# Optimization experiments

Measured on AMD Instinct MI355X. Metric: run time of the kernel, lower is better.

The kernel has to match this reference:

```python
import jax, jax.numpy as jnp
import numpy as np

N = 50000
E = 500000
F_IN = 128
H = 128
HEADS = 3
C = 10
G = 64
EPS = 1e-5
NEG_SLOPE = 0.2


def setup_inputs() -> dict:
    key = jax.random.key(0)
    ks = jax.random.split(key, 20)
    s = 0.1
    inp = {
        "x": jax.random.normal(ks[0], (N, F_IN), dtype=jnp.float32),
        "edge_index": jax.random.randint(ks[1], (2, E), 0, N, dtype=jnp.int64),
        "batch": jnp.sort(jax.random.randint(ks[2], (N,), 0, G, dtype=jnp.int64)),
        # GCNConv: lin weight + bias
        "W1": jax.random.normal(ks[3], (F_IN, H), dtype=jnp.float32) * s,
        "b1": jax.random.normal(ks[4], (H,), dtype=jnp.float32) * s,
        "gamma1": jnp.ones((H,), jnp.float32),
        "beta1": jnp.zeros((H,), jnp.float32),
        # SAGEConv: lin_l (neighbors, with bias) + lin_r (root, no bias)
        "Wl": jax.random.normal(ks[5], (H, H), dtype=jnp.float32) * s,
        "bl": jax.random.normal(ks[6], (H,), dtype=jnp.float32) * s,
        "Wr": jax.random.normal(ks[7], (H, H), dtype=jnp.float32) * s,
        "gamma2": jnp.ones((H,), jnp.float32),
        "beta2": jnp.zeros((H,), jnp.float32),
        # GATConv(heads=3, concat=False): lin + attention vectors + bias
        "W3": jax.random.normal(ks[8], (H, HEADS * H), dtype=jnp.float32) * s,
        "att_src": jax.random.normal(ks[9], (HEADS, H), dtype=jnp.float32) * s,
        "att_dst": jax.random.normal(ks[10], (HEADS, H), dtype=jnp.float32) * s,
        "b3": jax.random.normal(ks[11], (H,), dtype=jnp.float32) * s,
        "gamma3": jnp.ones((H,), jnp.float32),
        "beta3": jnp.zeros((H,), jnp.float32),
        # classifier
        "Wc": jax.random.normal(ks[12], (H, C), dtype=jnp.float32) * s,
        "bc": jax.random.normal(ks[13], (C,), dtype=jnp.float32) * s,
    }
    return inp


def _add_self_loops(src, dst):
    loop = jnp.arange(N, dtype=src.dtype)
    return jnp.concatenate([src, loop]), jnp.concatenate([dst, loop])


def _batch_norm(h, gamma, beta):
    mu = h.mean(axis=0)
    var = ((h - mu) ** 2).mean(axis=0)  # biased var, as torch BN training
    return (h - mu) * jax.lax.rsqrt(var + EPS) * gamma + beta


def gcn_conv(x, src, dst, W, b):
    s2, d2 = _add_self_loops(src, dst)
    deg = jax.ops.segment_sum(jnp.ones_like(d2, dtype=x.dtype), d2, num_segments=N)
    dinv = jnp.where(deg > 0, jax.lax.rsqrt(deg), 0.0)
    h = x @ W  # [N, H]
    norm = dinv[s2] * dinv[d2]  # [E+N]
    out = jax.ops.segment_sum(h[s2] * norm[:, None], d2, num_segments=N)
    return out + b


def sage_conv(x, src, dst, Wl, bl, Wr):
    # mean aggregation of neighbors + root transform
    deg = jax.ops.segment_sum(jnp.ones_like(dst, dtype=x.dtype), dst, num_segments=N)
    agg = jax.ops.segment_sum(x[src], dst, num_segments=N) / jnp.maximum(deg, 1.0)[:, None]
    return agg @ Wl + bl + x @ Wr


def gat_conv(x, src, dst, W, att_src, att_dst, b):
    s2, d2 = _add_self_loops(src, dst)
    h = (x @ W).reshape(N, HEADS, H)  # [N, heads, H]
    a_src = (h * att_src).sum(-1)  # [N, heads]
    a_dst = (h * att_dst).sum(-1)
    e = jax.nn.leaky_relu(a_src[s2] + a_dst[d2], NEG_SLOPE)  # [E2, heads]
    m = jax.ops.segment_max(e, d2, num_segments=N)  # stable softmax per target
    ex = jnp.exp(e - m[d2])
    denom = jax.ops.segment_sum(ex, d2, num_segments=N)
    alpha = ex / denom[d2]  # self-loops guarantee denom > 0
    out = jax.ops.segment_sum(h[s2] * alpha[:, :, None], d2, num_segments=N)
    return out.mean(axis=1) + b  # concat=False -> mean over heads


def reference(x, edge_index, batch, W1, b1, gamma1, beta1, Wl, bl, Wr,
              gamma2, beta2, W3, att_src, att_dst, b3, gamma3, beta3, Wc, bc):
    src, dst = edge_index[0], edge_index[1]
    h = jax.nn.elu(_batch_norm(gcn_conv(x, src, dst, W1, b1), gamma1, beta1))
    h = jax.nn.elu(_batch_norm(sage_conv(h, src, dst, Wl, bl, Wr), gamma2, beta2))
    h = jax.nn.elu(_batch_norm(gat_conv(h, src, dst, W3, att_src, att_dst, b3), gamma3, beta3))
    # global mean pool over graphs
    cnt = jax.ops.segment_sum(jnp.ones((N,), h.dtype), batch, num_segments=G)
    pooled = jax.ops.segment_sum(h, batch, num_segments=G) / jnp.maximum(cnt, 1.0)[:, None]
    logits = pooled @ Wc + bc
    return pooled, logits
```

## Files before the change

kernel.cpp:

```cpp
#include <hip/hip_runtime.h>
#include <math.h>

#define NN 50000
#define EE 500000
#define HH 128
#define NHEADS 3
#define CC 10
#define GG 64
#define EPSV 1e-5f
#define SLOPE 0.2f

typedef __attribute__((ext_vector_type(8))) short short8;
typedef __attribute__((ext_vector_type(4))) float f32x4;
typedef __attribute__((ext_vector_type(2))) float f32x2;


__device__ __forceinline__ unsigned short f2b(float x) {
    unsigned int u = __builtin_bit_cast(unsigned int, x);
    return (unsigned short)((u + 0x7fffu + ((u >> 16) & 1u)) >> 16);
}
__device__ __forceinline__ unsigned int pack2(float a, float b) {
    return (unsigned int)f2b(a) | ((unsigned int)f2b(b) << 16);
}
__device__ __forceinline__ float2 b2f2(unsigned int u) {
    float2 r;
    r.x = __builtin_bit_cast(float, u << 16);
    r.y = __builtin_bit_cast(float, u & 0xffff0000u);
    return r;
}


__global__ void k_zero(int* __restrict__ deg, float* __restrict__ bn1,
                       float* __restrict__ bn_sums23, float* __restrict__ poolacc) {
    int i = blockIdx.x * 256 + threadIdx.x;
    if (i < NN) deg[i] = 0;
    if (i < 256) bn1[i] = 0.f;
    if (i < 512) bn_sums23[i] = 0.f;
    if (i < GG * 128 + GG) poolacc[i] = 0.f;
}


__global__ void k_count_deg(const int* __restrict__ ei, int* __restrict__ deg) {
    int e = blockIdx.x * 256 + threadIdx.x;
    if (e < EE) atomicAdd(&deg[ei[EE + e]], 1);
}

__global__ void k_scan1(const int* __restrict__ deg, int* __restrict__ row_start,
                        int* __restrict__ blk) {
    __shared__ int s[256];
    int i = blockIdx.x * 256 + threadIdx.x;
    int v = (i < NN) ? deg[i] : 0;
    s[threadIdx.x] = v;
    __syncthreads();
    for (int o = 1; o < 256; o <<= 1) {
        int t = (threadIdx.x >= o) ? s[threadIdx.x - o] : 0;
        __syncthreads();
        s[threadIdx.x] += t;
        __syncthreads();
    }
    if (i < NN) row_start[i] = s[threadIdx.x] - v;
    if (threadIdx.x == 255) blk[blockIdx.x] = s[255];
}

__global__ void k_scan2(int* __restrict__ blk, int nb) {
    __shared__ int s[256];
    int v = (threadIdx.x < nb) ? blk[threadIdx.x] : 0;
    s[threadIdx.x] = v;
    __syncthreads();
    for (int o = 1; o < 256; o <<= 1) {
        int t = (threadIdx.x >= o) ? s[threadIdx.x - o] : 0;
        __syncthreads();
        s[threadIdx.x] += t;
        __syncthreads();
    }
    if (threadIdx.x < nb) blk[threadIdx.x] = s[threadIdx.x] - v;
}

__global__ void k_scan3(int* __restrict__ row_start, const int* __restrict__ blk,
                        const int* __restrict__ deg, int* __restrict__ cursor,
                        float* __restrict__ dinv, float* __restrict__ inv_sage) {
    int i = blockIdx.x * 256 + threadIdx.x;
    if (i < NN) {
        int rs = row_start[i] + blk[blockIdx.x];
        row_start[i] = rs;
        cursor[i] = rs;
        int d = deg[i];
        dinv[i] = rsqrtf((float)(d + 1));
        inv_sage[i] = 1.0f / (float)(d > 1 ? d : 1);
    }
}

__global__ void k_fill(const int* __restrict__ ei, int* __restrict__ cursor,
                       int* __restrict__ csr_src) {
    int e = blockIdx.x * 256 + threadIdx.x;
    if (e < EE) {
        int d = ei[EE + e];
        int p = atomicAdd(&cursor[d], 1);
        csr_src[p] = ei[e];
    }
}


__device__ __forceinline__ void split_store(float x, size_t dst, short* hi, short* lo) {
    unsigned int ux = __builtin_bit_cast(unsigned int, x);
    unsigned short hx = (unsigned short)(ux >> 16);
    float fx = __builtin_bit_cast(float, ux & 0xffff0000u);
    unsigned short lx = (unsigned short)(__builtin_bit_cast(unsigned int, x - fx) >> 16);
    hi[dst] = (short)hx;
    lo[dst] = (short)lx;
}

__device__ __forceinline__ void prep_one(float x, int k, int n, int cBase,
                                         short* hi, short* lo) {
    int c = (k >> 6) + cBase;
    int s = (k >> 5) & 1, quad = (k >> 3) & 3, j = k & 7;
    int G = n >> 4, l = quad * 16 + (n & 15);
    size_t dst = ((((size_t)(c * 2 + s)) * 8 + G) * 64 + l) * 8 + j;
    split_store(x, dst, hi, lo);
}

__global__ void k_prep_all(const float* __restrict__ W1, const float* __restrict__ Wl,
                           const float* __restrict__ Wr, const float* __restrict__ W3,
                           const float* __restrict__ att_src, const float* __restrict__ att_dst,
                           short* __restrict__ w1hi, short* __restrict__ w1lo,
                           short* __restrict__ wshi, short* __restrict__ wslo,
                           short* __restrict__ w3hi, short* __restrict__ w3lo,
                           float* __restrict__ wsrc, float* __restrict__ wdst) {
    int b = blockIdx.x, tid = threadIdx.x;
    if (b < 64) {
        int i = b * 256 + tid;
        prep_one(W1[i], i >> 7, i & 127, 0, w1hi, w1lo);
    } else if (b < 128) {
        int i = (b - 64) * 256 + tid;
        prep_one(Wl[i], i >> 7, i & 127, 0, wshi, wslo);
    } else if (b < 192) {
        int i = (b - 128) * 256 + tid;
        prep_one(Wr[i], i >> 7, i & 127, 2, wshi, wslo);
    } else if (b < 384) {
        int i = (b - 192) * 256 + tid;
        int k = i >> 7, n = i & 127;
        int h = k >> 7, kk = k & 127;
        float x = W3[(size_t)kk * 384 + h * 128 + n] * (1.f / 3.f);
        prep_one(x, k, n, 0, w3hi, w3lo);
    } else {
        for (int e = tid; e < 384; e += 256) {
            int h = e >> 7, k = e & 127;
            float s1 = 0.f, s2 = 0.f;
            const float* wrow = W3 + (size_t)k * 384 + h * 128;
            const float* as = att_src + h * 128;
            const float* ad = att_dst + h * 128;
            for (int j = 0; j < 128; j++) {
                float wv = wrow[j];
                s1 += wv * as[j];
                s2 += wv * ad[j];
            }
            wsrc[e] = s1;
            wdst[e] = s2;
        }
    }
}


template <bool ABF16, bool OUTB, bool STATS>
__global__ __launch_bounds__(256) void k_gemm_mfma(
    const void* __restrict__ A1v, const void* __restrict__ A2v,
    const short* __restrict__ Bhi, const short* __restrict__ Blo,
    const float* __restrict__ bias, void* __restrict__ Cv,
    float* __restrict__ sums, int M, int kc1, int kcT, int strideA1) {
    __shared__ short Ahi[128 * 72];
    __shared__ short Alo[ABF16 ? 8 : 128 * 72];
    __shared__ float cs[256];
    int tid = threadIdx.x;
    int rBase = blockIdx.x * 128;
    int wv = tid >> 6, lane = tid & 63;
    int rowHalf = wv >> 1, colHalf = wv & 1;
    int quad = lane >> 4, l15 = lane & 15;

    f32x4 acc[4][4];
#pragma unroll
    for (int a = 0; a < 4; a++)
#pragma unroll
        for (int b = 0; b < 4; b++) acc[a][b] = (f32x4)(0.f);

    for (int c = 0; c < kcT; c++) {
        const void* Asrc;
        int kOff, strideA;
        if (c < kc1) { Asrc = A1v; kOff = c * 64; strideA = strideA1; }
        else { Asrc = A2v; kOff = (c - kc1) * 64; strideA = 128; }

        __syncthreads();
        if (ABF16) {
            const unsigned short* As = (const unsigned short*)Asrc;
#pragma unroll
            for (int q = 0; q < 4; q++) {
                int slot = q * 256 + tid;
                int r = slot >> 3, k8 = slot & 7;
                uint4 v = make_uint4(0, 0, 0, 0);
                int gr = rBase + r;
                if (gr < M) v = *(const uint4*)(As + (size_t)gr * strideA + kOff + k8 * 8);
                *(uint4*)(Ahi + r * 72 + k8 * 8) = v;
            }
        } else {
            const float* As = (const float*)Asrc;
#pragma unroll
            for (int q8 = 0; q8 < 8; q8++) {
                int slot = q8 * 256 + tid;
                int r = slot >> 4, k4 = slot & 15;
                float4 v = make_float4(0.f, 0.f, 0.f, 0.f);
                int gr = rBase + r;
                if (gr < M) v = *(const float4*)(As + (size_t)gr * strideA + kOff + k4 * 4);
                unsigned int ux = __builtin_bit_cast(unsigned int, v.x);
                unsigned int uy = __builtin_bit_cast(unsigned int, v.y);
                unsigned int uz = __builtin_bit_cast(unsigned int, v.z);
                unsigned int uw = __builtin_bit_cast(unsigned int, v.w);
                unsigned int hx = ux >> 16, hy = uy >> 16, hz = uz >> 16, hw = uw >> 16;
                float fx = __builtin_bit_cast(float, ux & 0xffff0000u);
                float fy = __builtin_bit_cast(float, uy & 0xffff0000u);
                float fz = __builtin_bit_cast(float, uz & 0xffff0000u);
                float fw = __builtin_bit_cast(float, uw & 0xffff0000u);
                unsigned int lx = __builtin_bit_cast(unsigned int, v.x - fx) >> 16;
                unsigned int ly = __builtin_bit_cast(unsigned int, v.y - fy) >> 16;
                unsigned int lz = __builtin_bit_cast(unsigned int, v.z - fz) >> 16;
                unsigned int lw = __builtin_bit_cast(unsigned int, v.w - fw) >> 16;
                uint2 ph = make_uint2(hx | (hy << 16), hz | (hw << 16));
                uint2 pl = make_uint2(lx | (ly << 16), lz | (lw << 16));
                *(uint2*)(Ahi + r * 72 + k4 * 4) = ph;
                *(uint2*)(Alo + r * 72 + k4 * 4) = pl;
            }
        }
        __syncthreads();

#pragma unroll
        for (int s = 0; s < 2; s++) {
            short8 ah[4], al[4];
#pragma unroll
            for (int rb = 0; rb < 4; rb++) {
                int m = rowHalf * 64 + rb * 16 + l15;
                ah[rb] = *(const short8*)(Ahi + m * 72 + s * 32 + quad * 8);
                if (!ABF16) al[rb] = *(const short8*)(Alo + m * 72 + s * 32 + quad * 8);
            }
#pragma unroll
            for (int cg = 0; cg < 4; cg++) {
                int G = colHalf * 4 + cg;
                size_t bo = ((((size_t)(c * 2 + s)) * 8 + G) * 64 + lane) * 8;
                short8 bh = *(const short8*)(Bhi + bo);
                short8 bl = *(const short8*)(Blo + bo);
#pragma unroll
                for (int rb = 0; rb < 4; rb++) {
                    acc[rb][cg] = __builtin_amdgcn_mfma_f32_16x16x32_bf16(ah[rb], bh, acc[rb][cg], 0, 0, 0);
                    if (!ABF16)
                        acc[rb][cg] = __builtin_amdgcn_mfma_f32_16x16x32_bf16(al[rb], bh, acc[rb][cg], 0, 0, 0);
                    acc[rb][cg] = __builtin_amdgcn_mfma_f32_16x16x32_bf16(ah[rb], bl, acc[rb][cg], 0, 0, 0);
                }
            }
        }
    }

    if (STATS) {
        cs[tid] = 0.f;
        __syncthreads();
    }

#pragma unroll
    for (int cg = 0; cg < 4; cg++) {
        int col = colHalf * 64 + cg * 16 + l15;
        float bv = bias ? bias[col] : 0.f;
        float ps = 0.f, pq = 0.f;
#pragma unroll
        for (int rb = 0; rb < 4; rb++) {
#pragma unroll
            for (int r = 0; r < 4; r++) {
                int row = rBase + rowHalf * 64 + rb * 16 + quad * 4 + r;
                if (row < M) {
                    float ov = acc[rb][cg][r] + bv;
                    if (OUTB) ((unsigned short*)Cv)[(size_t)row * HH + col] = f2b(ov);
                    else ((float*)Cv)[(size_t)row * HH + col] = ov;
                    if (STATS) { ps += ov; pq += ov * ov; }
                }
            }
        }
        if (STATS) {
            ps += __shfl_xor(ps, 16, 64); ps += __shfl_xor(ps, 32, 64);
            pq += __shfl_xor(pq, 16, 64); pq += __shfl_xor(pq, 32, 64);
            if (quad == 0) {
                atomicAdd(&cs[col], ps);
                atomicAdd(&cs[128 + col], pq);
            }
        }
    }
    if (STATS) {
        __syncthreads();
        atomicAdd(&sums[tid], cs[tid]);
    }
}


__global__ void k_gcn_agg(const unsigned int* __restrict__ hb, const int* __restrict__ row_start,
                          const int* __restrict__ deg, const int* __restrict__ csr,
                          const float* __restrict__ dinv, const float* __restrict__ b1,
                          unsigned int* __restrict__ outb) {
    int tid = threadIdx.x;
    int n = blockIdx.x * 16 + (tid >> 4);
    if (n >= NN) return;
    int l = tid & 15;
    const uint4* hb4 = (const uint4*)hb;
    float di = dinv[n];
    float wsq = di * di;
    uint4 hv4 = hb4[(size_t)n * 16 + l];
    float2 p0 = b2f2(hv4.x), p1 = b2f2(hv4.y), p2 = b2f2(hv4.z), p3 = b2f2(hv4.w);
    float acc[8] = {p0.x * wsq, p0.y * wsq, p1.x * wsq, p1.y * wsq,
                    p2.x * wsq, p2.y * wsq, p3.x * wsq, p3.y * wsq};
    int s0 = row_start[n], cnt = deg[n];
    int i = 0;
    for (; i + 4 <= cnt; i += 4) {
        int ss[4]; float ww[4]; uint4 vv[4];
#pragma unroll
        for (int j = 0; j < 4; j++) ss[j] = csr[s0 + i + j];
#pragma unroll
        for (int j = 0; j < 4; j++) { ww[j] = dinv[ss[j]]; vv[j] = hb4[(size_t)ss[j] * 16 + l]; }
#pragma unroll
        for (int j = 0; j < 4; j++) {
            float wj = ww[j] * di;
            float2 q0 = b2f2(vv[j].x), q1 = b2f2(vv[j].y), q2 = b2f2(vv[j].z), q3 = b2f2(vv[j].w);
            acc[0] += q0.x * wj; acc[1] += q0.y * wj;
            acc[2] += q1.x * wj; acc[3] += q1.y * wj;
            acc[4] += q2.x * wj; acc[5] += q2.y * wj;
            acc[6] += q3.x * wj; acc[7] += q3.y * wj;
        }
    }
    for (; i < cnt; i++) {
        int s = csr[s0 + i];
        float wj = dinv[s] * di;
        uint4 v = hb4[(size_t)s * 16 + l];
        float2 q0 = b2f2(v.x), q1 = b2f2(v.y), q2 = b2f2(v.z), q3 = b2f2(v.w);
        acc[0] += q0.x * wj; acc[1] += q0.y * wj;
        acc[2] += q1.x * wj; acc[3] += q1.y * wj;
        acc[4] += q2.x * wj; acc[5] += q2.y * wj;
        acc[6] += q3.x * wj; acc[7] += q3.y * wj;
    }
    float4 bb0 = *(const float4*)(b1 + l * 8);
    float4 bb1 = *(const float4*)(b1 + l * 8 + 4);
    uint4 o;
    o.x = pack2(acc[0] + bb0.x, acc[1] + bb0.y);
    o.y = pack2(acc[2] + bb0.z, acc[3] + bb0.w);
    o.z = pack2(acc[4] + bb1.x, acc[5] + bb1.y);
    o.w = pack2(acc[6] + bb1.z, acc[7] + bb1.w);
    ((uint4*)outb)[(size_t)n * 16 + l] = o;
}


__global__ void k_bn_stats_b(const unsigned int* __restrict__ hb, float* __restrict__ sums) {
    int f = threadIdx.x;
    int rows_per = (NN + gridDim.x - 1) / gridDim.x;
    int r0 = blockIdx.x * rows_per;
    int r1 = r0 + rows_per;
    if (r1 > NN) r1 = NN;
    int wi = f >> 1, hi = f & 1;
    float s = 0.f, sq = 0.f;
    for (int r = r0; r < r1; r++) {
        float2 vv = b2f2(hb[(size_t)r * 64 + wi]);
        float v = hi ? vv.y : vv.x;
        s += v;
        sq += v * v;
    }
    atomicAdd(&sums[f], s);
    atomicAdd(&sums[128 + f], sq);
}


__global__ void k_sage_agg(const unsigned int* __restrict__ hb, const int* __restrict__ row_start,
                           const int* __restrict__ deg, const int* __restrict__ csr,
                           const float* __restrict__ inv_sage, unsigned int* __restrict__ outb) {
    int tid = threadIdx.x;
    int n = blockIdx.x * 16 + (tid >> 4);
    if (n >= NN) return;
    int l = tid & 15;
    const uint4* hb4 = (const uint4*)hb;
    float acc[8] = {0.f, 0.f, 0.f, 0.f, 0.f, 0.f, 0.f, 0.f};
    int s0 = row_start[n], cnt = deg[n];
    int i = 0;
    for (; i + 4 <= cnt; i += 4) {
        int ss[4]; uint4 vv[4];
#pragma unroll
        for (int j = 0; j < 4; j++) ss[j] = csr[s0 + i + j];
#pragma unroll
        for (int j = 0; j < 4; j++) vv[j] = hb4[(size_t)ss[j] * 16 + l];
#pragma unroll
        for (int j = 0; j < 4; j++) {
            float2 q0 = b2f2(vv[j].x), q1 = b2f2(vv[j].y), q2 = b2f2(vv[j].z), q3 = b2f2(vv[j].w);
            acc[0] += q0.x; acc[1] += q0.y;
            acc[2] += q1.x; acc[3] += q1.y;
            acc[4] += q2.x; acc[5] += q2.y;
            acc[6] += q3.x; acc[7] += q3.y;
        }
    }
    for (; i < cnt; i++) {
        uint4 v = hb4[(size_t)csr[s0 + i] * 16 + l];
        float2 q0 = b2f2(v.x), q1 = b2f2(v.y), q2 = b2f2(v.z), q3 = b2f2(v.w);
        acc[0] += q0.x; acc[1] += q0.y;
        acc[2] += q1.x; acc[3] += q1.y;
        acc[4] += q2.x; acc[5] += q2.y;
        acc[6] += q3.x; acc[7] += q3.y;
    }
    float sc = inv_sage[n];
    uint4 o;
    o.x = pack2(acc[0] * sc, acc[1] * sc);
    o.y = pack2(acc[2] * sc, acc[3] * sc);
    o.z = pack2(acc[4] * sc, acc[5] * sc);
    o.w = pack2(acc[6] * sc, acc[7] * sc);
    ((uint4*)outb)[(size_t)n * 16 + l] = o;
}


__device__ __forceinline__ float lrelu(float a) { return fmaxf(a, SLOPE * a); }

__global__ void k_gat_fused(const unsigned short* __restrict__ h8, const int* __restrict__ row_start,
                            const int* __restrict__ deg, const int* __restrict__ csr,
                            const float4* __restrict__ asrc4, const float4* __restrict__ adst4,
                            float4* __restrict__ alphaE, unsigned int* __restrict__ aggb) {
    int n = blockIdx.x * 4 + (threadIdx.x >> 6);
    if (n >= NN) return;
    int lane = threadIdx.x & 63;
    float4 ad = adst4[n], asv = asrc4[n];
    float es0 = lrelu(asv.x + ad.x), es1 = lrelu(asv.y + ad.y), es2 = lrelu(asv.z + ad.z);
    int s0 = row_start[n], cnt = deg[n];
    float self0, self1, self2;
    unsigned int pk1 = 0, pk2 = 0;
    bool fast = (cnt <= 64);
    if (fast) {
        bool valid = lane < cnt;
        int sReg = 0;
        float e0 = -3e38f, e1 = -3e38f, e2 = -3e38f;
        if (valid) {
            sReg = csr[s0 + lane];
            float4 a4 = asrc4[sReg];
            e0 = lrelu(a4.x + ad.x); e1 = lrelu(a4.y + ad.y); e2 = lrelu(a4.z + ad.z);
        }
        float M0 = e0, M1 = e1, M2 = e2;
#pragma unroll
        for (int o = 32; o > 0; o >>= 1) {
            M0 = fmaxf(M0, __shfl_xor(M0, o, 64));
            M1 = fmaxf(M1, __shfl_xor(M1, o, 64));
            M2 = fmaxf(M2, __shfl_xor(M2, o, 64));
        }
        float m0 = fmaxf(es0, M0), m1 = fmaxf(es1, M1), m2 = fmaxf(es2, M2);
        float w0 = valid ? __expf(e0 - m0) : 0.f;
        float w1 = valid ? __expf(e1 - m1) : 0.f;
        float w2 = valid ? __expf(e2 - m2) : 0.f;
        float S0 = w0, S1 = w1, S2 = w2;
#pragma unroll
        for (int o = 32; o > 0; o >>= 1) {
            S0 += __shfl_xor(S0, o, 64);
            S1 += __shfl_xor(S1, o, 64);
            S2 += __shfl_xor(S2, o, 64);
        }
        float sw0 = __expf(es0 - m0), sw1 = __expf(es1 - m1), sw2 = __expf(es2 - m2);
        float r0 = 1.f / (S0 + sw0), r1 = 1.f / (S1 + sw1), r2 = 1.f / (S2 + sw2);
        pk1 = ((unsigned int)sReg & 0xffffu) | ((unsigned int)f2b(w2 * r2) << 16);
        pk2 = pack2(w0 * r0, w1 * r1);
        self0 = sw0 * r0; self1 = sw1 * r1; self2 = sw2 * r2;
    } else {
        float m0 = es0, m1 = es1, m2 = es2;
        for (int base = 0; base < cnt; base += 64) {
            int i2 = base + lane;
            float e0 = -3e38f, e1 = -3e38f, e2 = -3e38f;
            if (i2 < cnt) {
                int s = csr[s0 + i2];
                float4 a4 = asrc4[s];
                e0 = lrelu(a4.x + ad.x); e1 = lrelu(a4.y + ad.y); e2 = lrelu(a4.z + ad.z);
                alphaE[s0 + i2] = make_float4(e0, e1, e2, 0.f);
            }
#pragma unroll
            for (int o = 32; o > 0; o >>= 1) {
                e0 = fmaxf(e0, __shfl_xor(e0, o, 64));
                e1 = fmaxf(e1, __shfl_xor(e1, o, 64));
                e2 = fmaxf(e2, __shfl_xor(e2, o, 64));
            }
            m0 = fmaxf(m0, e0); m1 = fmaxf(m1, e1); m2 = fmaxf(m2, e2);
        }
        float l0 = __expf(es0 - m0), l1 = __expf(es1 - m1), l2 = __expf(es2 - m2);
        for (int base = 0; base < cnt; base += 64) {
            int i2 = base + lane;
            float w0 = 0.f, w1 = 0.f, w2 = 0.f;
            if (i2 < cnt) {
                float4 e = alphaE[s0 + i2];
                w0 = __expf(e.x - m0); w1 = __expf(e.y - m1); w2 = __expf(e.z - m2);
            }
#pragma unroll
            for (int o = 32; o > 0; o >>= 1) {
                w0 += __shfl_xor(w0, o, 64);
                w1 += __shfl_xor(w1, o, 64);
                w2 += __shfl_xor(w2, o, 64);
            }
            l0 += w0; l1 += w1; l2 += w2;
        }
        float r0 = 1.f / l0, r1 = 1.f / l1, r2 = 1.f / l2;
        self0 = __expf(es0 - m0) * r0;
        self1 = __expf(es1 - m1) * r1;
        self2 = __expf(es2 - m2) * r2;
        for (int base = 0; base < cnt; base += 64) {
            int i2 = base + lane;
            if (i2 < cnt) {
                float4 e = alphaE[s0 + i2];
                alphaE[s0 + i2] = make_float4(__expf(e.x - m0) * r0, __expf(e.y - m1) * r1,
                                              __expf(e.z - m2) * r2, 0.f);
            }
        }
    }

    f32x2 hv = __builtin_amdgcn_cvt_pk_f32_fp8((int)h8[(size_t)n * 64 + lane], false);
    float2 a0 = make_float2(hv.x * self0, hv.y * self0);
    float2 a1 = make_float2(hv.x * self1, hv.y * self1);
    float2 a2 = make_float2(hv.x * self2, hv.y * self2);
    if (fast) {
        int i = 0;
        for (; i + 4 <= cnt; i += 4) {
            unsigned int q1[4], q2[4]; unsigned short uu[4];
#pragma unroll
            for (int j = 0; j < 4; j++) {
                q1[j] = __shfl(pk1, i + j, 64);
                q2[j] = __shfl(pk2, i + j, 64);
            }
#pragma unroll
            for (int j = 0; j < 4; j++) uu[j] = h8[(size_t)(q1[j] & 0xffffu) * 64 + lane];
#pragma unroll
            for (int j = 0; j < 4; j++) {
                f32x2 v = __builtin_amdgcn_cvt_pk_f32_fp8((int)uu[j], false);
                float2 a01 = b2f2(q2[j]);
                float w2 = __builtin_bit_cast(float, q1[j] & 0xffff0000u);
                a0.x += a01.x * v.x; a0.y += a01.x * v.y;
                a1.x += a01.y * v.x; a1.y += a01.y * v.y;
                a2.x += w2 * v.x;    a2.y += w2 * v.y;
            }
        }
        for (; i < cnt; i++) {
            unsigned int q1 = __shfl(pk1, i, 64);
            unsigned int q2 = __shfl(pk2, i, 64);
            f32x2 v = __builtin_amdgcn_cvt_pk_f32_fp8((int)h8[(size_t)(q1 & 0xffffu) * 64 + lane], false);
            float2 a01 = b2f2(q2);
            float w2 = __builtin_bit_cast(float, q1 & 0xffff0000u);
            a0.x += a01.x * v.x; a0.y += a01.x * v.y;
            a1.x += a01.y * v.x; a1.y += a01.y * v.y;
            a2.x += w2 * v.x;    a2.y += w2 * v.y;
        }
    } else {
        for (int i = 0; i < cnt; i++) {
            int s = csr[s0 + i];
            float4 al = alphaE[s0 + i];
            f32x2 v = __builtin_amdgcn_cvt_pk_f32_fp8((int)h8[(size_t)s * 64 + lane], false);
            a0.x += al.x * v.x; a0.y += al.x * v.y;
            a1.x += al.y * v.x; a1.y += al.y * v.y;
            a2.x += al.z * v.x; a2.y += al.z * v.y;
        }
    }
    unsigned int* op = aggb + (size_t)n * 192;
    op[lane] = pack2(a0.x, a0.y);
    op[64 + lane] = pack2(a1.x, a1.y);
    op[128 + lane] = pack2(a2.x, a2.y);
}


__device__ __forceinline__ float elu1(float x) { return x > 0.f ? x : (__expf(x) - 1.f); }

__device__ __forceinline__ float4 bn_apply4(float4 v, const float* sums,
                                            const float* gamma, const float* beta, int f4) {
    const float invN = 1.0f / NN;
    float4 s4 = *(const float4*)(sums + f4);
    float4 q4 = *(const float4*)(sums + 128 + f4);
    float4 g4 = *(const float4*)(gamma + f4);
    float4 b4 = *(const float4*)(beta + f4);
    float mx = s4.x * invN, my = s4.y * invN, mz = s4.z * invN, mw = s4.w * invN;
    float scx = rsqrtf(q4.x * invN - mx * mx + EPSV) * g4.x;
    float scy = rsqrtf(q4.y * invN - my * my + EPSV) * g4.y;
    float scz = rsqrtf(q4.z * invN - mz * mz + EPSV) * g4.z;
    float scw = rsqrtf(q4.w * invN - mw * mw + EPSV) * g4.w;
    v.x = elu1(v.x * scx + (b4.x - mx * scx));
    v.y = elu1(v.y * scy + (b4.y - my * scy));
    v.z = elu1(v.z * scz + (b4.z - mz * scz));
    v.w = elu1(v.w * scw + (b4.w - mw * scw));
    return v;
}

__global__ void k_bn_elu_b(const unsigned int* __restrict__ hpre, const float* __restrict__ sums,
                           const float* __restrict__ gamma, const float* __restrict__ beta,
                           unsigned int* __restrict__ hb) {
    int i = blockIdx.x * 256 + threadIdx.x;
    int f4 = (i & 31) << 2;
    uint2 p = *(const uint2*)(hpre + (size_t)(i >> 5) * 64 + (i & 31) * 2);
    float2 v01 = b2f2(p.x), v23 = b2f2(p.y);
    float4 v = make_float4(v01.x, v01.y, v23.x, v23.y);
    v = bn_apply4(v, sums, gamma, beta, f4);
    uint2 q = make_uint2(pack2(v.x, v.y), pack2(v.z, v.w));
    *(uint2*)(hb + (size_t)(i >> 5) * 64 + (i & 31) * 2) = q;
}

__global__ void k_bn_elu_att(const float* __restrict__ h, const float* __restrict__ sums,
                             const float* __restrict__ gamma, const float* __restrict__ beta,
                             const float* __restrict__ wsrc, const float* __restrict__ wdst,
                             unsigned int* __restrict__ h8w, float4* __restrict__ asrc4,
                             float4* __restrict__ adst4) {
    int i = blockIdx.x * 256 + threadIdx.x;
    int fi = i & 31;
    int f4 = fi << 2;
    float4 v = bn_apply4(((const float4*)h)[i], sums, gamma, beta, f4);
    int p8 = __builtin_amdgcn_cvt_pk_fp8_f32(v.x, v.y, 0, false);
    p8 = __builtin_amdgcn_cvt_pk_fp8_f32(v.z, v.w, p8, true);
    h8w[(size_t)(i >> 5) * 32 + fi] = (unsigned int)p8;
    const float4* ws4 = (const float4*)wsrc;
    const float4* wd4 = (const float4*)wdst;
    float d[6];
#pragma unroll
    for (int hd = 0; hd < 3; hd++) {
        float4 a = ws4[hd * 32 + fi];
        float4 b = wd4[hd * 32 + fi];
        d[hd] = v.x * a.x + v.y * a.y + v.z * a.z + v.w * a.w;
        d[3 + hd] = v.x * b.x + v.y * b.y + v.z * b.z + v.w * b.w;
    }
#pragma unroll
    for (int o = 16; o > 0; o >>= 1) {
#pragma unroll
        for (int j = 0; j < 6; j++) d[j] += __shfl_xor(d[j], o, 64);
    }
    if ((threadIdx.x & 31) == 0) {
        int r = i >> 5;
        asrc4[r] = make_float4(d[0], d[1], d[2], 0.f);
        adst4[r] = make_float4(d[3], d[4], d[5], 0.f);
    }
}


#define POOL_BLOCKS 800

__global__ void k_pool_bn(const unsigned int* __restrict__ hb, const int* __restrict__ batch,
                          const float* __restrict__ sums, const float* __restrict__ gamma,
                          const float* __restrict__ beta, float* __restrict__ pool,
                          float* __restrict__ cntf) {
    const int RP = (NN + POOL_BLOCKS - 1) / POOL_BLOCKS;
    int r0 = blockIdx.x * RP;
    int r1 = r0 + RP;
    if (r1 > NN) r1 = NN;
    if (r0 >= r1) return;
    int f = threadIdx.x;
    const float invN = 1.0f / NN;
    float mu = sums[f] * invN;
    float var = sums[128 + f] * invN - mu * mu;
    float sc = rsqrtf(var + EPSV) * gamma[f];
    float sh = beta[f] - mu * sc;
    int g = batch[r0];
    float s = 0.f, c = 0.f;
    for (int r = r0; r < r1; r++) {
        int gr = batch[r];
        if (gr != g) {
            atomicAdd(&pool[g * 128 + f], s);
            if (f == 0) atomicAdd(&cntf[g], c);
            s = 0.f; c = 0.f; g = gr;
        }
        unsigned int u = hb[(size_t)r * 64 + (f >> 1)];
        float2 vv = b2f2(u);
        float hv = (f & 1) ? vv.y : vv.x;
        s += elu1(hv * sc + sh);
        c += 1.f;
    }
    atomicAdd(&pool[g * 128 + f], s);
    if (f == 0) atomicAdd(&cntf[g], c);
}

__global__ void k_pool_fin(const float* __restrict__ pool, const float* __restrict__ cntf,
                           const float* __restrict__ Wc, const float* __restrict__ bc,
                           float* __restrict__ outp) {
    __shared__ float pr[128];
    int g = blockIdx.x, f = threadIdx.x;
    float c = fmaxf(cntf[g], 1.f);
    float pv = pool[g * 128 + f] / c;
    outp[g * 128 + f] = pv;
    pr[f] = pv;
    __syncthreads();
    if (f < CC) {
        float s = bc[f];
        for (int k = 0; k < 128; k++) s += pr[k] * Wc[k * CC + f];
        outp[GG * HH + g * CC + f] = s;
    }
}


extern "C" void kernel_launch(void* const* d_in, const int* in_sizes, int n_in,
                              void* d_out, int out_size, void* d_ws, size_t ws_size,
                              hipStream_t stream) {
    const float* x = (const float*)d_in[0];
    const int* ei = (const int*)d_in[1];
    const int* batch = (const int*)d_in[2];
    const float* W1 = (const float*)d_in[3];
    const float* b1 = (const float*)d_in[4];
    const float* gamma1 = (const float*)d_in[5];
    const float* beta1 = (const float*)d_in[6];
    const float* Wl = (const float*)d_in[7];
    const float* bl = (const float*)d_in[8];
    const float* Wr = (const float*)d_in[9];
    const float* gamma2 = (const float*)d_in[10];
    const float* beta2 = (const float*)d_in[11];
    const float* W3 = (const float*)d_in[12];
    const float* att_src = (const float*)d_in[13];
    const float* att_dst = (const float*)d_in[14];
    const float* b3 = (const float*)d_in[15];
    const float* gamma3 = (const float*)d_in[16];
    const float* beta3 = (const float*)d_in[17];
    const float* Wc = (const float*)d_in[18];
    const float* bc = (const float*)d_in[19];

    char* w = (char*)d_ws;
    size_t o = 0;
    float* bufC = (float*)(w + o); o += (size_t)NN * 128 * 4;
    unsigned int* h0b = (unsigned int*)(w + o); o += (size_t)NN * 128 * 2;
    unsigned int* h1pre = (unsigned int*)(w + o); o += (size_t)NN * 128 * 2;
    unsigned int* h1b = (unsigned int*)(w + o); o += (size_t)NN * 128 * 2;
    unsigned int* sageb = (unsigned int*)(w + o); o += (size_t)NN * 128 * 2;
    unsigned int* h2f8 = (unsigned int*)(w + o); o += (size_t)NN * 128;
    unsigned int* aggDb = (unsigned int*)(w + o); o += (size_t)NN * 384 * 2;
    unsigned int* h3b = (unsigned int*)(w + o); o += (size_t)NN * 128 * 2;
    int* csr = (int*)(w + o); o += (size_t)EE * 4;
    int* deg = (int*)(w + o); o += (size_t)NN * 4;
    int* row_start = (int*)(w + o); o += (size_t)NN * 4;
    int* cursor = (int*)(w + o); o += (size_t)NN * 4;
    float* dinv = (float*)(w + o); o += (size_t)NN * 4;
    float* inv_sage = (float*)(w + o); o += (size_t)NN * 4;
    float4* asrc4 = (float4*)(w + o); o += (size_t)NN * 16;
    float4* adst4 = (float4*)(w + o); o += (size_t)NN * 16;
    float* bn1 = (float*)(w + o); o += 256 * 4;
    float* bn_sums23 = (float*)(w + o); o += 512 * 4;
    int* blk = (int*)(w + o); o += 1024;
    float* poolacc = (float*)(w + o); o += (size_t)GG * 128 * 4;
    float* cntf = (float*)(w + o); o += (size_t)GG * 4;
    float* wsrc = (float*)(w + o); o += 384 * 4;
    float* wdst = (float*)(w + o); o += 384 * 4;
    float4* alphaE = (float4*)(w + o); o += (size_t)EE * 16;
    short* w1hi = (short*)(w + o); o += (size_t)128 * 128 * 2;
    short* w1lo = (short*)(w + o); o += (size_t)128 * 128 * 2;
    short* wshi = (short*)(w + o); o += (size_t)256 * 128 * 2;
    short* wslo = (short*)(w + o); o += (size_t)256 * 128 * 2;
    short* w3hi = (short*)(w + o); o += (size_t)384 * 128 * 2;
    short* w3lo = (short*)(w + o); o += (size_t)384 * 128 * 2;

    float* outp = (float*)d_out;

    const int NB_SCAN = (NN + 255) / 256;
    const int EB = (EE + 255) / 256;
    const int NW4 = (NN + 3) / 4;
    const int NG16 = (NN + 15) / 16;
    const int GB = (NN + 127) / 128;

    k_zero<<<NB_SCAN, 256, 0, stream>>>(deg, bn1, bn_sums23, poolacc);
    k_count_deg<<<EB, 256, 0, stream>>>(ei, deg);
    k_scan1<<<NB_SCAN, 256, 0, stream>>>(deg, row_start, blk);
    k_scan2<<<1, 256, 0, stream>>>(blk, NB_SCAN);
    k_scan3<<<NB_SCAN, 256, 0, stream>>>(row_start, blk, deg, cursor, dinv, inv_sage);
    k_fill<<<EB, 256, 0, stream>>>(ei, cursor, csr);
    k_prep_all<<<385, 256, 0, stream>>>(W1, Wl, Wr, W3, att_src, att_dst, w1hi, w1lo,
                                        wshi, wslo, w3hi, w3lo, wsrc, wdst);

    k_gemm_mfma<false, true, false><<<GB, 256, 0, stream>>>(x, nullptr, w1hi, w1lo, nullptr,
                                                            h0b, nullptr, NN, 2, 2, 128);
    k_gcn_agg<<<NG16, 256, 0, stream>>>(h0b, row_start, deg, csr, dinv, b1, h1pre);
    k_bn_stats_b<<<1024, 128, 0, stream>>>(h1pre, bn1);
    k_bn_elu_b<<<NN * 32 / 256, 256, 0, stream>>>(h1pre, bn1, gamma1, beta1, h1b);

    k_sage_agg<<<NG16, 256, 0, stream>>>(h1b, row_start, deg, csr, inv_sage, sageb);
    k_gemm_mfma<true, false, true><<<GB, 256, 0, stream>>>(sageb, h1b, wshi, wslo, bl, bufC,
                                                           bn_sums23, NN, 2, 4, 128);
    k_bn_elu_att<<<NN * 32 / 256, 256, 0, stream>>>(bufC, bn_sums23, gamma2, beta2,
                                                    wsrc, wdst, h2f8, asrc4, adst4);

    k_gat_fused<<<NW4, 256, 0, stream>>>((const unsigned short*)h2f8, row_start, deg, csr,
                                         asrc4, adst4, alphaE, aggDb);
    k_gemm_mfma<true, true, true><<<GB, 256, 0, stream>>>(aggDb, nullptr, w3hi, w3lo, b3, h3b,
                                                          bn_sums23 + 256, NN, 6, 6, 384);

    k_pool_bn<<<POOL_BLOCKS, 128, 0, stream>>>(h3b, batch, bn_sums23 + 256, gamma3, beta3,
                                               poolacc, cntf);
    k_pool_fin<<<GG, 128, 0, stream>>>(poolacc, cntf, Wc, bc, outp);
}
```

Baseline: 435.4 us.

## Map two GAT target nodes per wavefront with 4-byte fp8 loads per lane

```diff
diff --git a/kernel.cpp b/kernel.cpp
--- a/kernel.cpp
+++ b/kernel.cpp
@@ -414,31 +414,33 @@
 
 __device__ __forceinline__ float lrelu(float a) { return fmaxf(a, SLOPE * a); }
 
-__global__ void k_gat_fused(const unsigned short* __restrict__ h8, const int* __restrict__ row_start,
+__global__ void k_gat_fused(const unsigned int* __restrict__ h8u, const int* __restrict__ row_start,
                             const int* __restrict__ deg, const int* __restrict__ csr,
                             const float4* __restrict__ asrc4, const float4* __restrict__ adst4,
                             float4* __restrict__ alphaE, unsigned int* __restrict__ aggb) {
-    int n = blockIdx.x * 4 + (threadIdx.x >> 6);
+    int tid = threadIdx.x;
+    int wv = tid >> 6, lane = tid & 63;
+    int half = lane >> 5, l = lane & 31;
+    int n = blockIdx.x * 8 + wv * 2 + half;
     if (n >= NN) return;
-    int lane = threadIdx.x & 63;
     float4 ad = adst4[n], asv = asrc4[n];
     float es0 = lrelu(asv.x + ad.x), es1 = lrelu(asv.y + ad.y), es2 = lrelu(asv.z + ad.z);
     int s0 = row_start[n], cnt = deg[n];
     float self0, self1, self2;
     unsigned int pk1 = 0, pk2 = 0;
-    bool fast = (cnt <= 64);
+    bool fast = (cnt <= 32);
     if (fast) {
-        bool valid = lane < cnt;
+        bool valid = l < cnt;
         int sReg = 0;
         float e0 = -3e38f, e1 = -3e38f, e2 = -3e38f;
         if (valid) {
-            sReg = csr[s0 + lane];
+            sReg = csr[s0 + l];
             float4 a4 = asrc4[sReg];
             e0 = lrelu(a4.x + ad.x); e1 = lrelu(a4.y + ad.y); e2 = lrelu(a4.z + ad.z);
         }
         float M0 = e0, M1 = e1, M2 = e2;
 #pragma unroll
-        for (int o = 32; o > 0; o >>= 1) {
+        for (int o = 16; o > 0; o >>= 1) {
             M0 = fmaxf(M0, __shfl_xor(M0, o, 64));
             M1 = fmaxf(M1, __shfl_xor(M1, o, 64));
             M2 = fmaxf(M2, __shfl_xor(M2, o, 64));
@@ -449,7 +451,7 @@
         float w2 = valid ? __expf(e2 - m2) : 0.f;
         float S0 = w0, S1 = w1, S2 = w2;
 #pragma unroll
-        for (int o = 32; o > 0; o >>= 1) {
+        for (int o = 16; o > 0; o >>= 1) {
             S0 += __shfl_xor(S0, o, 64);
             S1 += __shfl_xor(S1, o, 64);
             S2 += __shfl_xor(S2, o, 64);
@@ -461,8 +463,8 @@
         self0 = sw0 * r0; self1 = sw1 * r1; self2 = sw2 * r2;
     } else {
         float m0 = es0, m1 = es1, m2 = es2;
-        for (int base = 0; base < cnt; base += 64) {
-            int i2 = base + lane;
+        for (int base = 0; base < cnt; base += 32) {
+            int i2 = base + l;
             float e0 = -3e38f, e1 = -3e38f, e2 = -3e38f;
             if (i2 < cnt) {
                 int s = csr[s0 + i2];
@@ -471,7 +473,7 @@
                 alphaE[s0 + i2] = make_float4(e0, e1, e2, 0.f);
             }
 #pragma unroll
-            for (int o = 32; o > 0; o >>= 1) {
+            for (int o = 16; o > 0; o >>= 1) {
                 e0 = fmaxf(e0, __shfl_xor(e0, o, 64));
                 e1 = fmaxf(e1, __shfl_xor(e1, o, 64));
                 e2 = fmaxf(e2, __shfl_xor(e2, o, 64));
@@ -479,15 +481,15 @@
             m0 = fmaxf(m0, e0); m1 = fmaxf(m1, e1); m2 = fmaxf(m2, e2);
         }
         float l0 = __expf(es0 - m0), l1 = __expf(es1 - m1), l2 = __expf(es2 - m2);
-        for (int base = 0; base < cnt; base += 64) {
-            int i2 = base + lane;
+        for (int base = 0; base < cnt; base += 32) {
+            int i2 = base + l;
             float w0 = 0.f, w1 = 0.f, w2 = 0.f;
             if (i2 < cnt) {
                 float4 e = alphaE[s0 + i2];
                 w0 = __expf(e.x - m0); w1 = __expf(e.y - m1); w2 = __expf(e.z - m2);
             }
 #pragma unroll
-            for (int o = 32; o > 0; o >>= 1) {
+            for (int o = 16; o > 0; o >>= 1) {
                 w0 += __shfl_xor(w0, o, 64);
                 w1 += __shfl_xor(w1, o, 64);
                 w2 += __shfl_xor(w2, o, 64);
@@ -498,8 +500,8 @@
         self0 = __expf(es0 - m0) * r0;
         self1 = __expf(es1 - m1) * r1;
         self2 = __expf(es2 - m2) * r2;
-        for (int base = 0; base < cnt; base += 64) {
-            int i2 = base + lane;
+        for (int base = 0; base < cnt; base += 32) {
+            int i2 = base + l;
             if (i2 < cnt) {
                 float4 e = alphaE[s0 + i2];
                 alphaE[s0 + i2] = make_float4(__expf(e.x - m0) * r0, __expf(e.y - m1) * r1,
@@ -508,55 +510,63 @@
         }
     }
 
-    f32x2 hv = __builtin_amdgcn_cvt_pk_f32_fp8((int)h8[(size_t)n * 64 + lane], false);
-    float2 a0 = make_float2(hv.x * self0, hv.y * self0);
-    float2 a1 = make_float2(hv.x * self1, hv.y * self1);
-    float2 a2 = make_float2(hv.x * self2, hv.y * self2);
+    unsigned int hvu = h8u[(size_t)n * 32 + l];
+    f32x2 v01 = __builtin_amdgcn_cvt_pk_f32_fp8((int)hvu, false);
+    f32x2 v23 = __builtin_amdgcn_cvt_pk_f32_fp8((int)hvu, true);
+    f32x2 a0l = v01 * self0, a0h = v23 * self0;
+    f32x2 a1l = v01 * self1, a1h = v23 * self1;
+    f32x2 a2l = v01 * self2, a2h = v23 * self2;
+    int lbase = half << 5;
     if (fast) {
         int i = 0;
         for (; i + 4 <= cnt; i += 4) {
-            unsigned int q1[4], q2[4]; unsigned short uu[4];
+            unsigned int q1[4], q2[4], uu[4];
 #pragma unroll
             for (int j = 0; j < 4; j++) {
-                q1[j] = __shfl(pk1, i + j, 64);
-                q2[j] = __shfl(pk2, i + j, 64);
-            }
-#pragma unroll
-            for (int j = 0; j < 4; j++) uu[j] = h8[(size_t)(q1[j] & 0xffffu) * 64 + lane];
+                q1[j] = __shfl(pk1, lbase + i + j, 64);
+                q2[j] = __shfl(pk2, lbase + i + j, 64);
+            }
+#pragma unroll
+            for (int j = 0; j < 4; j++) uu[j] = h8u[(size_t)(q1[j] & 0xffffu) * 32 + l];
 #pragma unroll
             for (int j = 0; j < 4; j++) {
-                f32x2 v = __builtin_amdgcn_cvt_pk_f32_fp8((int)uu[j], false);
+                f32x2 w01 = __builtin_amdgcn_cvt_pk_f32_fp8((int)uu[j], false);
+                f32x2 w23 = __builtin_amdgcn_cvt_pk_f32_fp8((int)uu[j], true);
                 float2 a01 = b2f2(q2[j]);
                 float w2 = __builtin_bit_cast(float, q1[j] & 0xffff0000u);
-                a0.x += a01.x * v.x; a0.y += a01.x * v.y;
-                a1.x += a01.y * v.x; a1.y += a01.y * v.y;
-                a2.x += w2 * v.x;    a2.y += w2 * v.y;
+                a0l += a01.x * w01; a0h += a01.x * w23;
+                a1l += a01.y * w01; a1h += a01.y * w23;
+                a2l += w2 * w01;    a2h += w2 * w23;
             }
         }
         for (; i < cnt; i++) {
-            unsigned int q1 = __shfl(pk1, i, 64);
-            unsigned int q2 = __shfl(pk2, i, 64);
-            f32x2 v = __builtin_amdgcn_cvt_pk_f32_fp8((int)h8[(size_t)(q1 & 0xffffu) * 64 + lane], false);
+            unsigned int q1 = __shfl(pk1, lbase + i, 64);
+            unsigned int q2 = __shfl(pk2, lbase + i, 64);
+            unsigned int u = h8u[(size_t)(q1 & 0xffffu) * 32 + l];
+            f32x2 w01 = __builtin_amdgcn_cvt_pk_f32_fp8((int)u, false);
+            f32x2 w23 = __builtin_amdgcn_cvt_pk_f32_fp8((int)u, true);
             float2 a01 = b2f2(q2);
             float w2 = __builtin_bit_cast(float, q1 & 0xffff0000u);
-            a0.x += a01.x * v.x; a0.y += a01.x * v.y;
-            a1.x += a01.y * v.x; a1.y += a01.y * v.y;
-            a2.x += w2 * v.x;    a2.y += w2 * v.y;
+            a0l += a01.x * w01; a0h += a01.x * w23;
+            a1l += a01.y * w01; a1h += a01.y * w23;
+            a2l += w2 * w01;    a2h += w2 * w23;
         }
     } else {
         for (int i = 0; i < cnt; i++) {
             int s = csr[s0 + i];
             float4 al = alphaE[s0 + i];
-            f32x2 v = __builtin_amdgcn_cvt_pk_f32_fp8((int)h8[(size_t)s * 64 + lane], false);
-            a0.x += al.x * v.x; a0.y += al.x * v.y;
-            a1.x += al.y * v.x; a1.y += al.y * v.y;
-            a2.x += al.z * v.x; a2.y += al.z * v.y;
-        }
-    }
-    unsigned int* op = aggb + (size_t)n * 192;
-    op[lane] = pack2(a0.x, a0.y);
-    op[64 + lane] = pack2(a1.x, a1.y);
-    op[128 + lane] = pack2(a2.x, a2.y);
+            unsigned int u = h8u[(size_t)s * 32 + l];
+            f32x2 w01 = __builtin_amdgcn_cvt_pk_f32_fp8((int)u, false);
+            f32x2 w23 = __builtin_amdgcn_cvt_pk_f32_fp8((int)u, true);
+            a0l += al.x * w01; a0h += al.x * w23;
+            a1l += al.y * w01; a1h += al.y * w23;
+            a2l += al.z * w01; a2h += al.z * w23;
+        }
+    }
+    unsigned int* op = aggb + (size_t)n * 192 + 2 * l;
+    *(uint2*)(op) = make_uint2(pack2(a0l.x, a0l.y), pack2(a0h.x, a0h.y));
+    *(uint2*)(op + 64) = make_uint2(pack2(a1l.x, a1l.y), pack2(a1h.x, a1h.y));
+    *(uint2*)(op + 128) = make_uint2(pack2(a2l.x, a2l.y), pack2(a2h.x, a2h.y));
 }
 
 
@@ -744,7 +754,7 @@
 
     const int NB_SCAN = (NN + 255) / 256;
     const int EB = (EE + 255) / 256;
-    const int NW4 = (NN + 3) / 4;
+    const int NG8 = (NN + 7) / 8;
     const int NG16 = (NN + 15) / 16;
     const int GB = (NN + 127) / 128;
 
@@ -769,8 +779,7 @@
     k_bn_elu_att<<<NN * 32 / 256, 256, 0, stream>>>(bufC, bn_sums23, gamma2, beta2,
                                                     wsrc, wdst, h2f8, asrc4, adst4);
 
-    k_gat_fused<<<NW4, 256, 0, stream>>>((const unsigned short*)h2f8, row_start, deg, csr,
-                                         asrc4, adst4, alphaE, aggDb);
+    k_gat_fused<<<NG8, 256, 0, stream>>>(h2f8, row_start, deg, csr, asrc4, adst4, alphaE, aggDb);
     k_gemm_mfma<true, true, true><<<GB, 256, 0, stream>>>(aggDb, nullptr, w3hi, w3lo, b3, h3b,
                                                           bn_sums23 + 256, NN, 6, 6, 384);
 
```

Measured after the change: 421.9 us. 1.03x faster.
